# Kernel optimization log

Hardware: AMD Instinct MI355X
Metric: run time of the kernel (lower is better)

The kernel has to match this reference:

```python
import jax, jax.numpy as jnp
import numpy as np

B, S, D, H = 2, 2048, 1024, 16
DK = D // H


def setup_inputs() -> dict:
    key = jax.random.key(0)
    ks = jax.random.split(key, 12)
    s = 0.02
    return {
        "q": jax.random.normal(ks[0], (B, S, D), jnp.float32),
        "k": jax.random.normal(ks[1], (B, S, D), jnp.float32),
        "v": jax.random.normal(ks[2], (B, S, D), jnp.float32),
        "mask": jax.random.randint(ks[3], (1, 1, S, S), 0, 2, jnp.int32),
        "Wq": jax.random.normal(ks[4], (D, D), jnp.float32) * s,
        "bq": jnp.zeros((D,), jnp.float32),
        "Wk": jax.random.normal(ks[5], (D, D), jnp.float32) * s,
        "bk": jnp.zeros((D,), jnp.float32),
        "Wv": jax.random.normal(ks[6], (D, D), jnp.float32) * s,
        "bv": jnp.zeros((D,), jnp.float32),
        "Wo": jax.random.normal(ks[7], (D, D), jnp.float32) * s,
        "bo": jnp.zeros((D,), jnp.float32),
    }


def reference(q, k, v, mask, Wq, bq, Wk, bk, Wv, bv, Wo, bo):
    # linear projections (torch Linear: x @ W.T + b)
    qp = q @ Wq.T + bq
    kp = k @ Wk.T + bk
    vp = v @ Wv.T + bv
    # [B, S, D] -> [B, H, S, DK]
    split = lambda x: x.reshape(B, S, H, DK).transpose(0, 2, 1, 3)
    qh, kh, vh = split(qp), split(kp), split(vp)
    scale = 1.0 / jnp.sqrt(jnp.float32(DK))
    attn = jnp.einsum('bhsd,bhtd->bhst', qh, kh) * scale  # [B,H,S,S]
    attn = jnp.where(mask == 0, jnp.float32(-1e9), attn)
    attn = jax.nn.softmax(attn, axis=-1)
    out = jnp.einsum('bhst,bhtd->bhsd', attn, vh)  # [B,H,S,DK]
    concat = out.transpose(0, 2, 1, 3).reshape(B, S, D)
    return concat @ Wo.T + bo
```

## Files before the change

kernel.cpp:

```cpp
#include <hip/hip_runtime.h>
#include <hip/hip_bf16.h>


using bf16x8 = __attribute__((ext_vector_type(8))) short;
using f32x4  = __attribute__((ext_vector_type(4))) float;

constexpr int Bc = 2, Sc = 2048, Dc = 1024, Hc = 16, DKc = 64;
constexpr int Mc = Bc * Sc;
#define QSCALE 0.18033688011112042f

__device__ __forceinline__ void lds_load16(const void* g, void* l) {
  __builtin_amdgcn_global_load_lds(
      (const __attribute__((address_space(1))) unsigned int*)g,
      (__attribute__((address_space(3))) unsigned int*)l, 16, 0, 0);
}

#if __has_builtin(__builtin_amdgcn_exp2f)
__device__ __forceinline__ float exp2_fast(float x) { return __builtin_amdgcn_exp2f(x); }
#else
__device__ __forceinline__ float exp2_fast(float x) {
  float r;
  asm("v_exp_f32 %0, %1\n\ts_nop 0" : "=v"(r) : "v"(x));
  return r;
}
#endif

__device__ __forceinline__ unsigned pack_trunc(float a, float b) {
  return __builtin_amdgcn_perm(__float_as_uint(b), __float_as_uint(a), 0x07060302u);
}

__device__ __forceinline__ unsigned pack2bf(float a, float b) {
  union { __hip_bfloat16 h; unsigned short s; } ua, ub;
  ua.h = __float2bfloat16(a);
  ub.h = __float2bfloat16(b);
  return (unsigned)ua.s | ((unsigned)ub.s << 16);
}

__global__ void prep(const float* __restrict__ q, const float* __restrict__ k,
                     const float* __restrict__ v, const int* __restrict__ mask,
                     const float* __restrict__ Wq, const float* __restrict__ Wk,
                     const float* __restrict__ Wv, const float* __restrict__ Wo,
                     char* __restrict__ ws) {
  const size_t MB = 1024 * 1024;
  int blk = blockIdx.x;
  if (blk < 12288) {
    int which = blk >> 12;
    int i = (((blk & 4095) << 8) + threadIdx.x) * 4;
    const float* s = which == 0 ? q : (which == 1 ? k : v);
    __hip_bfloat16* d = (__hip_bfloat16*)(ws + (size_t)which * 8 * MB);
    float4 x = *(const float4*)&s[i];
    uint2 pk = {pack2bf(x.x, x.y), pack2bf(x.z, x.w)};
    *(uint2*)&d[i] = pk;
  } else if (blk < 16384) {
    int bb = blk - 12288;
    int which = bb >> 10;
    int i = (((bb & 1023) << 8) + threadIdx.x) * 4;
    const float* s = which == 0 ? Wq : (which == 1 ? Wk : (which == 2 ? Wv : Wo));
    __hip_bfloat16* d = which < 3 ? (__hip_bfloat16*)(ws + (24 + 2 * which) * MB)
                                  : (__hip_bfloat16*)(ws + 30 * MB);
    float4 x = *(const float4*)&s[i];
    uint2 pk = {pack2bf(x.x, x.y), pack2bf(x.z, x.w)};
    *(uint2*)&d[i] = pk;
  } else {
    int i = ((blk - 16384) << 8) + threadIdx.x;
    unsigned long long bal = __ballot(mask[i] != 0);
    if ((threadIdx.x & 63) == 0)
      ((unsigned long long*)(ws + 32 * MB))[i >> 6] = bal;
  }
}

__global__ __launch_bounds__(256, 3) void proj_qkv(
    const __hip_bfloat16* __restrict__ qb, const __hip_bfloat16* __restrict__ kb,
    const __hip_bfloat16* __restrict__ vb, const __hip_bfloat16* __restrict__ Wcat,
    const float* __restrict__ bq, const float* __restrict__ bk,
    const float* __restrict__ bv, __hip_bfloat16* __restrict__ qhd,
    __hip_bfloat16* __restrict__ khd, __hip_bfloat16* __restrict__ vtd) {
  __shared__ __align__(16) __hip_bfloat16 As[2][128 * 32];
  __shared__ __align__(16) __hip_bfloat16 Bs[2][128 * 32];
  const int tid = threadIdx.x;
  const int f = blockIdx.x, g = f >> 3;
  const int m0 = ((f & 7) * 4 + g / 24) * 128;
  const int n0 = (g % 24) * 128;
  const int which = n0 >> 10, nl0 = n0 & 1023;
  const __hip_bfloat16* X = which == 0 ? qb : (which == 1 ? kb : vb);
  const float* bias = which == 0 ? bq : (which == 1 ? bk : bv);
  const int w = tid >> 6, lane = tid & 63, ln = lane & 15, quad = lane >> 4;
  const int rl = w * 32 + (lane >> 2);
  const int sw8 = ((lane & 3) ^ ((lane >> 2) & 3)) * 8;
  const int aoff = (n0 + rl) * 1024 + sw8;
  const int boff = (m0 + rl) * 1024 + sw8;
  char* aDst = (char*)As + w * 2048 + lane * 16;
  char* bDst = (char*)Bs + w * 2048 + lane * 16;
  const int rkq = (quad ^ (ln & 3)) * 16;
  const int rA0 = ((w >> 1) * 64 + ln) * 64 + rkq;
  const int rB0 = ((w & 1) * 64 + ln) * 64 + rkq;
  f32x4 acc[4][4] = {};

#define PSTAGE(KO, BI)                                                        \
  {                                                                           \
    lds_load16(&Wcat[aoff + (KO)], aDst + (BI)*8192);                         \
    lds_load16(&Wcat[aoff + 16384 + (KO)], aDst + (BI)*8192 + 1024);          \
    lds_load16(&X[boff + (KO)], bDst + (BI)*8192);                            \
    lds_load16(&X[boff + 16384 + (KO)], bDst + (BI)*8192 + 1024);             \
  }

  PSTAGE(0, 0);
  if (which == 2) {
    for (int kb32 = 0; kb32 < 32; ++kb32) {
      const int bi = kb32 & 1;
      __syncthreads();
      if (kb32 < 31) PSTAGE((kb32 + 1) * 32, bi ^ 1);
      bf16x8 af[4], bf[4];
#pragma unroll
      for (int i = 0; i < 4; ++i)
        af[i] = *(bf16x8*)((char*)As + bi * 8192 + rA0 + i * 1024);
#pragma unroll
      for (int j = 0; j < 4; ++j)
        bf[j] = *(bf16x8*)((char*)Bs + bi * 8192 + rB0 + j * 1024);
#pragma unroll
      for (int i = 0; i < 4; ++i)
#pragma unroll
        for (int j = 0; j < 4; ++j)
          acc[i][j] = __builtin_amdgcn_mfma_f32_16x16x32_bf16(bf[j], af[i],
                                                              acc[i][j], 0, 0, 0);
    }
  } else {
    for (int kb32 = 0; kb32 < 32; ++kb32) {
      const int bi = kb32 & 1;
      __syncthreads();
      if (kb32 < 31) PSTAGE((kb32 + 1) * 32, bi ^ 1);
      bf16x8 af[4], bf[4];
#pragma unroll
      for (int i = 0; i < 4; ++i)
        af[i] = *(bf16x8*)((char*)As + bi * 8192 + rA0 + i * 1024);
#pragma unroll
      for (int j = 0; j < 4; ++j)
        bf[j] = *(bf16x8*)((char*)Bs + bi * 8192 + rB0 + j * 1024);
#pragma unroll
      for (int i = 0; i < 4; ++i)
#pragma unroll
        for (int j = 0; j < 4; ++j)
          acc[i][j] = __builtin_amdgcn_mfma_f32_16x16x32_bf16(af[i], bf[j],
                                                              acc[i][j], 0, 0, 0);
    }
  }

  const int wA = (w >> 1) * 64, wB = (w & 1) * 64;
  if (which == 2) {
#pragma unroll
    for (int i = 0; i < 4; ++i) {
      int nf = nl0 + wA + i * 16 + ln;
      int h = nf >> 6, dk = nf & 63;
      float bb = bias[nf];
#pragma unroll
      for (int j = 0; j < 4; ++j) {
        int sb = m0 + wB + j * 16 + quad * 4;
        int b = sb >> 11, s = sb & 2047;
        float vv[4] = {acc[i][j][0] + bb, acc[i][j][1] + bb,
                       acc[i][j][2] + bb, acc[i][j][3] + bb};
        uint2 pk = {pack2bf(vv[0], vv[1]), pack2bf(vv[2], vv[3])};
        *(uint2*)&vtd[(((size_t)(b * Hc + h) * DKc + dk) * Sc) + s] = pk;
      }
    }
  } else {
#pragma unroll
    for (int i = 0; i < 4; ++i) {
      int nfb = nl0 + wA + i * 16 + quad * 4;
      float4 b4 = *(const float4*)&bias[nfb];
      int h = nfb >> 6, dk0 = nfb & 63;
#pragma unroll
      for (int j = 0; j < 4; ++j) {
        int sg = m0 + wB + j * 16 + ln;
        int b = sg >> 11, s = sg & 2047;
        float vv[4] = {acc[i][j][0] + b4.x, acc[i][j][1] + b4.y,
                       acc[i][j][2] + b4.z, acc[i][j][3] + b4.w};
        if (which == 0) {
          uint2 pk = {pack2bf(vv[0] * QSCALE, vv[1] * QSCALE),
                      pack2bf(vv[2] * QSCALE, vv[3] * QSCALE)};
          *(uint2*)&qhd[(((size_t)(b * Hc + h) * Sc + s) * DKc) + dk0] = pk;
        } else {
          uint2 pk = {pack2bf(vv[0], vv[1]), pack2bf(vv[2], vv[3])};
          *(uint2*)&khd[(((size_t)(b * Hc + h) * Sc + s) * DKc) + dk0] = pk;
        }
      }
    }
  }
}

__global__ __launch_bounds__(256, 2) void gemm_out(
    const __hip_bfloat16* __restrict__ X, const __hip_bfloat16* __restrict__ W,
    const float* __restrict__ bias, float* __restrict__ Y) {
  __shared__ __align__(16) __hip_bfloat16 As[2][64 * 64];
  __shared__ __align__(16) __hip_bfloat16 Bs[2][128 * 64];
  const int tid = threadIdx.x;
  const int f = blockIdx.x, g = f >> 3;
  const int m0 = ((f & 7) * 4 + (g >> 4)) * 128;
  const int n0 = (g & 15) * 64;
  const int w = tid >> 6, lane = tid & 63, ln = lane & 15, quad = lane >> 4;
  const int wA = (w & 1) * 32, wB = (w >> 1) * 64;
  const int swz = ((lane & 7) ^ (lane >> 3)) * 8;
  const int rk0 = ln * 128 + ((quad ^ (ln & 7)) * 16);
  const int rk1 = ln * 128 + (((quad + 4) ^ (ln & 7)) * 16);
  const int aoff = (n0 + w * 16 + (lane >> 3)) * 1024 + swz;
  const int boff = (m0 + w * 32 + (lane >> 3)) * 1024 + swz;
  f32x4 acc[2][4] = {};

#define OSTAGE(KO, BI)                                                        \
  {                                                                           \
    _Pragma("unroll") for (int i = 0; i < 2; ++i)                             \
        lds_load16(&W[aoff + i * 8192 + (KO)],                                \
                   (char*)As[BI] + w * 2048 + lane * 16 + i * 1024);          \
    _Pragma("unroll") for (int i = 0; i < 4; ++i)                             \
        lds_load16(&X[boff + i * 8192 + (KO)],                                \
                   (char*)Bs[BI] + w * 4096 + lane * 16 + i * 1024);          \
  }

  OSTAGE(0, 0);
  for (int kb64 = 0; kb64 < 16; ++kb64) {
    const int bi = kb64 & 1;
    __syncthreads();
    if (kb64 + 1 < 16) OSTAGE((kb64 + 1) * 64, bi ^ 1);
    bf16x8 af[2][2], bf[4][2];
#pragma unroll
    for (int i = 0; i < 2; ++i) {
      af[i][0] = *(bf16x8*)((char*)As[bi] + wA * 128 + i * 2048 + rk0);
      af[i][1] = *(bf16x8*)((char*)As[bi] + wA * 128 + i * 2048 + rk1);
    }
#pragma unroll
    for (int j = 0; j < 4; ++j) {
      bf[j][0] = *(bf16x8*)((char*)Bs[bi] + wB * 128 + j * 2048 + rk0);
      bf[j][1] = *(bf16x8*)((char*)Bs[bi] + wB * 128 + j * 2048 + rk1);
    }
#pragma unroll
    for (int i = 0; i < 2; ++i)
#pragma unroll
      for (int j = 0; j < 4; ++j) {
        acc[i][j] = __builtin_amdgcn_mfma_f32_16x16x32_bf16(af[i][0], bf[j][0],
                                                            acc[i][j], 0, 0, 0);
        acc[i][j] = __builtin_amdgcn_mfma_f32_16x16x32_bf16(af[i][1], bf[j][1],
                                                            acc[i][j], 0, 0, 0);
      }
  }
#pragma unroll
  for (int i = 0; i < 2; ++i) {
    int nfb = n0 + wA + i * 16 + quad * 4;
    float4 b4 = *(const float4*)&bias[nfb];
#pragma unroll
    for (int j = 0; j < 4; ++j) {
      int sg = m0 + wB + j * 16 + ln;
      float4 st = {acc[i][j][0] + b4.x, acc[i][j][1] + b4.y,
                   acc[i][j][2] + b4.z, acc[i][j][3] + b4.w};
      *(float4*)&Y[(size_t)sg * Dc + nfb] = st;
    }
  }
}

__global__ __launch_bounds__(512, 4) void flash_attn(
    const __hip_bfloat16* __restrict__ qh, const __hip_bfloat16* __restrict__ kh,
    const __hip_bfloat16* __restrict__ vt, const uint4* __restrict__ mb4,
    __hip_bfloat16* __restrict__ oc) {
  __shared__ __align__(16) char L[51200];
  const int tid = threadIdx.x;
  const int f = blockIdx.x, g = f >> 3;
  const int bh = (f & 7) * 4 + (g >> 4);
  const int q0 = (g & 15) * 128;
  const int b = bh >> 4, h = bh & 15;
  const int w = tid >> 6, lane = tid & 63, ln = lane & 15, quad = lane >> 4;
  const int qg = w >> 1, kg = w & 1;
  const size_t base = (size_t)bh * Sc * DKc;
  const __hip_bfloat16* khb = kh + base;
  const __hip_bfloat16* vtb = vt + base;

  bf16x8 qf[2][2];
#pragma unroll
  for (int qt = 0; qt < 2; ++qt)
#pragma unroll
    for (int kc = 0; kc < 2; ++kc)
      qf[qt][kc] = *(const bf16x8*)&qh[base +
          (size_t)(q0 + qg * 32 + qt * 16 + ln) * 64 + kc * 32 + quad * 8];

  bf16x8 onesA;
#pragma unroll
  for (int i = 0; i < 8; ++i) onesA[i] = (short)0x3F80;

  const int swz = ((lane & 7) ^ (lane >> 3)) * 8;
  const int rk0 = ln * 128 + ((quad ^ (ln & 7)) * 16);
  const int rk1 = ln * 128 + (((quad + 4) ^ (ln & 7)) * 16);
  const int rkv = ln * 128 + ((((kg << 2) + quad) ^ (ln & 7)) * 16);
  const int rPw = 32768 + qg * 4608 + ln * 144 + kg * 64 + quad * 8;
  const int rPb = 32768 + qg * 4608 + ln * 144 + kg * 64 + quad * 16;
  char* dmaL = L + w * 1024 + lane * 16;
  int koff = (w * 8 + (lane >> 3)) * 64 + swz;
  int voff = (w * 8 + (lane >> 3)) * Sc + swz;
  int midx0 = (q0 + qg * 32 + ln) * 16;
  int midx1 = midx0 + 256;
  const int sh0 = quad * 4, sh1 = quad * 4 + 16;

#define KV_DMA(BI)                                                            \
  {                                                                           \
    lds_load16(khb + koff, dmaL + (BI)*8192);                                 \
    lds_load16(vtb + voff, dmaL + 16384 + (BI)*8192);                         \
  }

  f32x4 Oacc[4][2] = {};
  f32x4 lacc[2] = {};
  KV_DMA(0);

#define FTILE(BUF, E0, E1)                                                    \
  {                                                                           \
    bf16x8 kf[2][2];                                                          \
    _Pragma("unroll") for (int tl = 0; tl < 2; ++tl) {                        \
      kf[tl][0] = *(bf16x8*)(L + (BUF)*8192 + (kg * 2 + tl) * 2048 + rk0);    \
      kf[tl][1] = *(bf16x8*)(L + (BUF)*8192 + (kg * 2 + tl) * 2048 + rk1);    \
    }                                                                         \
    _Pragma("unroll") for (int qt = 0; qt < 2; ++qt) {                        \
      f32x4 s4[2];                                                            \
      __builtin_amdgcn_s_setprio(1);                                          \
      _Pragma("unroll") for (int tl = 0; tl < 2; ++tl) {                      \
        f32x4 z = {0.f, 0.f, 0.f, 0.f};                                       \
        z = __builtin_amdgcn_mfma_f32_16x16x32_bf16(kf[tl][0], qf[qt][0], z,  \
                                                    0, 0, 0);                 \
        s4[tl] = __builtin_amdgcn_mfma_f32_16x16x32_bf16(kf[tl][1],           \
                                                         qf[qt][1], z, 0, 0, 0); \
      }                                                                       \
      __builtin_amdgcn_s_setprio(0);                                          \
      unsigned word = qt ? (E1) : (E0);                                       \
      _Pragma("unroll") for (int tl = 0; tl < 2; ++tl) {                      \
        unsigned pre = word >> (tl ? sh1 : sh0);                              \
        float p[4];                                                           \
        _Pragma("unroll") for (int r = 0; r < 4; ++r) {                       \
          float e = exp2_fast(s4[tl][r]);                                     \
          p[r] = (pre & (1u << r)) ? e : 0.f;                                 \
        }                                                                     \
        uint2 pk = {pack_trunc(p[0], p[1]), pack_trunc(p[2], p[3])};          \
        *(uint2*)(L + rPw + qt * 2304 + tl * 32) = pk;                        \
      }                                                                       \
    }                                                                         \
    bf16x8 vf[4], pb[2];                                                      \
    _Pragma("unroll") for (int dt = 0; dt < 4; ++dt)                          \
        vf[dt] = *(bf16x8*)(L + 16384 + (BUF)*8192 + dt * 2048 + rkv);        \
    _Pragma("unroll") for (int qt = 0; qt < 2; ++qt)                          \
        pb[qt] = *(bf16x8*)(L + rPb + qt * 2304);                             \
    __builtin_amdgcn_s_setprio(1);                                            \
    _Pragma("unroll") for (int qt = 0; qt < 2; ++qt)                          \
        lacc[qt] = __builtin_amdgcn_mfma_f32_16x16x32_bf16(onesA, pb[qt],     \
                                                           lacc[qt], 0, 0, 0); \
    _Pragma("unroll") for (int dt = 0; dt < 4; ++dt)                          \
        _Pragma("unroll") for (int qt = 0; qt < 2; ++qt)                      \
            Oacc[dt][qt] = __builtin_amdgcn_mfma_f32_16x16x32_bf16(           \
                vf[dt], pb[qt], Oacc[dt][qt], 0, 0, 0);                       \
    __builtin_amdgcn_s_setprio(0);                                            \
  }

  for (int it2 = 0; it2 < 16; ++it2) {
    __syncthreads();
    uint4 mq0 = mb4[midx0], mq1 = mb4[midx1];
    ++midx0; ++midx1;
    koff += 4096; voff += 64;
    KV_DMA(1);
    FTILE(0, kg ? mq0.y : mq0.x, kg ? mq1.y : mq1.x);
    __syncthreads();
    if (it2 < 15) {
      koff += 4096; voff += 64;
      KV_DMA(0);
    }
    FTILE(1, kg ? mq0.w : mq0.z, kg ? mq1.w : mq1.z);
  }

  __syncthreads();
  if (kg) {
#pragma unroll
    for (int dt = 0; dt < 4; ++dt)
#pragma unroll
      for (int qt = 0; qt < 2; ++qt) {
        int slot = (dt * 4 + quad) ^ ln;
        *(f32x4*)(L + qg * 8192 + (qt * 16 + ln) * 256 + slot * 16) =
            Oacc[dt][qt];
      }
    if (quad == 0) {
      *(float*)(L + 32768 + qg * 4608 + ln * 144 + 128) = lacc[0][0];
      *(float*)(L + 32768 + qg * 4608 + 2304 + ln * 144 + 128) = lacc[1][0];
    }
  }
  __syncthreads();
  if (!kg) {
    float linv[2];
#pragma unroll
    for (int qt = 0; qt < 2; ++qt) {
      float lsum = lacc[qt][0] +
                   *(float*)(L + 32768 + qg * 4608 + qt * 2304 + ln * 144 + 128);
      linv[qt] = 1.f / fmaxf(lsum, 1e-30f);
    }
#pragma unroll
    for (int dt = 0; dt < 4; ++dt)
#pragma unroll
      for (int qt = 0; qt < 2; ++qt) {
        int slot = (dt * 4 + quad) ^ ln;
        f32x4 part =
            *(f32x4*)(L + qg * 8192 + (qt * 16 + ln) * 256 + slot * 16);
        f32x4 o = Oacc[dt][qt];
        o[0] += part[0]; o[1] += part[1]; o[2] += part[2]; o[3] += part[3];
        uint2 pk = {pack2bf(o[0] * linv[qt], o[1] * linv[qt]),
                    pack2bf(o[2] * linv[qt], o[3] * linv[qt])};
        *(uint2*)(L + rPw + qt * 2304 + dt * 32) = pk;
      }
    __builtin_amdgcn_s_waitcnt(0);
#pragma unroll
    for (int chunk = 0; chunk < 4; ++chunk) {
      int row = chunk * 8 + (lane >> 3);
      bf16x8 val =
          *(bf16x8*)(L + 32768 + qg * 4608 + row * 144 + (lane & 7) * 16);
      int s = q0 + qg * 32 + row;
      *(bf16x8*)&oc[(size_t)(b * Sc + s) * Dc + h * 64 + (lane & 7) * 8] = val;
    }
  }
#undef KV_DMA
#undef FTILE
}

extern "C" void kernel_launch(void* const* d_in, const int* in_sizes, int n_in,
                              void* d_out, int out_size, void* d_ws, size_t ws_size,
                              hipStream_t stream) {
  const float* q  = (const float*)d_in[0];
  const float* k  = (const float*)d_in[1];
  const float* v  = (const float*)d_in[2];
  const int* mask = (const int*)d_in[3];
  const float* Wq = (const float*)d_in[4];
  const float* bq = (const float*)d_in[5];
  const float* Wk = (const float*)d_in[6];
  const float* bk = (const float*)d_in[7];
  const float* Wv = (const float*)d_in[8];
  const float* bv = (const float*)d_in[9];
  const float* Wo = (const float*)d_in[10];
  const float* bo = (const float*)d_in[11];

  char* ws = (char*)d_ws;
  const size_t MB = 1024 * 1024;
  __hip_bfloat16* qb   = (__hip_bfloat16*)(ws + 0 * MB);
  __hip_bfloat16* kb   = (__hip_bfloat16*)(ws + 8 * MB);
  __hip_bfloat16* vb   = (__hip_bfloat16*)(ws + 16 * MB);
  __hip_bfloat16* Wcat = (__hip_bfloat16*)(ws + 24 * MB);
  __hip_bfloat16* Wob  = (__hip_bfloat16*)(ws + 30 * MB);
  uint4*          mb4  = (uint4*)(ws + 32 * MB);
  __hip_bfloat16* qhd  = (__hip_bfloat16*)(ws + 33 * MB);
  __hip_bfloat16* khd  = (__hip_bfloat16*)(ws + 41 * MB);
  __hip_bfloat16* vtd  = (__hip_bfloat16*)(ws + 49 * MB);
  __hip_bfloat16* oc   = (__hip_bfloat16*)(ws + 57 * MB);

  prep<<<32768, 256, 0, stream>>>(q, k, v, mask, Wq, Wk, Wv, Wo, ws);
  proj_qkv<<<768, 256, 0, stream>>>(qb, kb, vb, Wcat, bq, bk, bv, qhd, khd, vtd);
  flash_attn<<<512, 512, 0, stream>>>(qhd, khd, vtd, mb4, oc);
  gemm_out<<<512, 256, 0, stream>>>(oc, Wob, bo, (float*)d_out);
}
```

Before: 244.7 us.

## Triple-buffer K/V tiles in flash attention with two-deep async prefetch

```diff
diff --git a/kernel.cpp b/kernel.cpp
--- a/kernel.cpp
+++ b/kernel.cpp
@@ -259,7 +259,7 @@
     const __hip_bfloat16* __restrict__ qh, const __hip_bfloat16* __restrict__ kh,
     const __hip_bfloat16* __restrict__ vt, const uint4* __restrict__ mb4,
     __hip_bfloat16* __restrict__ oc) {
-  __shared__ __align__(16) char L[51200];
+  __shared__ __align__(16) char L[67584];
   const int tid = threadIdx.x;
   const int f = blockIdx.x, g = f >> 3;
   const int bh = (f & 7) * 4 + (g >> 4);
@@ -287,8 +287,8 @@
   const int rk0 = ln * 128 + ((quad ^ (ln & 7)) * 16);
   const int rk1 = ln * 128 + (((quad + 4) ^ (ln & 7)) * 16);
   const int rkv = ln * 128 + ((((kg << 2) + quad) ^ (ln & 7)) * 16);
-  const int rPw = 32768 + qg * 4608 + ln * 144 + kg * 64 + quad * 8;
-  const int rPb = 32768 + qg * 4608 + ln * 144 + kg * 64 + quad * 16;
+  const int rPw = 49152 + qg * 4608 + ln * 144 + kg * 64 + quad * 8;
+  const int rPb = 49152 + qg * 4608 + ln * 144 + kg * 64 + quad * 16;
   char* dmaL = L + w * 1024 + lane * 16;
   int koff = (w * 8 + (lane >> 3)) * 64 + swz;
   int voff = (w * 8 + (lane >> 3)) * Sc + swz;
@@ -296,22 +296,33 @@
   int midx1 = midx0 + 256;
   const int sh0 = quad * 4, sh1 = quad * 4 + 16;
 
-#define KV_DMA(BI)                                                            \
-  {                                                                           \
-    lds_load16(khb + koff, dmaL + (BI)*8192);                                 \
-    lds_load16(vtb + voff, dmaL + 16384 + (BI)*8192);                         \
+#define KV_DMA(BOFF)                                                          \
+  {                                                                           \
+    lds_load16(khb + koff, dmaL + (BOFF));                                    \
+    lds_load16(vtb + voff, dmaL + 24576 + (BOFF));                            \
+    koff += 4096; voff += 64;                                                 \
+  }
+
+#define WB2()                                                                 \
+  {                                                                           \
+    asm volatile("s_waitcnt vmcnt(2)" ::: "memory");                          \
+    __builtin_amdgcn_s_barrier();                                             \
+  }
+#define WB0()                                                                 \
+  {                                                                           \
+    asm volatile("s_waitcnt vmcnt(0)" ::: "memory");                          \
+    __builtin_amdgcn_s_barrier();                                             \
   }
 
   f32x4 Oacc[4][2] = {};
   f32x4 lacc[2] = {};
-  KV_DMA(0);
-
-#define FTILE(BUF, E0, E1)                                                    \
+
+#define FTILE(COFF, E0, E1)                                                   \
   {                                                                           \
     bf16x8 kf[2][2];                                                          \
     _Pragma("unroll") for (int tl = 0; tl < 2; ++tl) {                        \
-      kf[tl][0] = *(bf16x8*)(L + (BUF)*8192 + (kg * 2 + tl) * 2048 + rk0);    \
-      kf[tl][1] = *(bf16x8*)(L + (BUF)*8192 + (kg * 2 + tl) * 2048 + rk1);    \
+      kf[tl][0] = *(bf16x8*)(L + (COFF) + (kg * 2 + tl) * 2048 + rk0);        \
+      kf[tl][1] = *(bf16x8*)(L + (COFF) + (kg * 2 + tl) * 2048 + rk1);        \
     }                                                                         \
     _Pragma("unroll") for (int qt = 0; qt < 2; ++qt) {                        \
       f32x4 s4[2];                                                            \
@@ -338,7 +349,7 @@
     }                                                                         \
     bf16x8 vf[4], pb[2];                                                      \
     _Pragma("unroll") for (int dt = 0; dt < 4; ++dt)                          \
-        vf[dt] = *(bf16x8*)(L + 16384 + (BUF)*8192 + dt * 2048 + rkv);        \
+        vf[dt] = *(bf16x8*)(L + 24576 + (COFF) + dt * 2048 + rkv);            \
     _Pragma("unroll") for (int qt = 0; qt < 2; ++qt)                          \
         pb[qt] = *(bf16x8*)(L + rPb + qt * 2304);                             \
     __builtin_amdgcn_s_setprio(1);                                            \
@@ -352,19 +363,33 @@
     __builtin_amdgcn_s_setprio(0);                                            \
   }
 
+  uint4 mqC0 = mb4[midx0], mqC1 = mb4[midx1];
+  ++midx0; ++midx1;
+  KV_DMA(0);
+  KV_DMA(8192);
+  int curoff = 0, preoff = 16384;
+
   for (int it2 = 0; it2 < 16; ++it2) {
-    __syncthreads();
-    uint4 mq0 = mb4[midx0], mq1 = mb4[midx1];
-    ++midx0; ++midx1;
-    koff += 4096; voff += 64;
-    KV_DMA(1);
-    FTILE(0, kg ? mq0.y : mq0.x, kg ? mq1.y : mq1.x);
-    __syncthreads();
+    uint4 mqN0, mqN1;
+    WB2();
     if (it2 < 15) {
-      koff += 4096; voff += 64;
-      KV_DMA(0);
-    }
-    FTILE(1, kg ? mq0.w : mq0.z, kg ? mq1.w : mq1.z);
+      mqN0 = mb4[midx0]; mqN1 = mb4[midx1];
+      ++midx0; ++midx1;
+      KV_DMA(preoff);
+      preoff = preoff == 16384 ? 0 : preoff + 8192;
+    }
+    FTILE(curoff, kg ? mqC0.y : mqC0.x, kg ? mqC1.y : mqC1.x);
+    curoff = curoff == 16384 ? 0 : curoff + 8192;
+    if (it2 < 15) {
+      WB2();
+      KV_DMA(preoff);
+      preoff = preoff == 16384 ? 0 : preoff + 8192;
+    } else {
+      WB0();
+    }
+    FTILE(curoff, kg ? mqC0.w : mqC0.z, kg ? mqC1.w : mqC1.z);
+    curoff = curoff == 16384 ? 0 : curoff + 8192;
+    if (it2 < 15) { mqC0 = mqN0; mqC1 = mqN1; }
   }
 
   __syncthreads();
@@ -378,8 +403,8 @@
             Oacc[dt][qt];
       }
     if (quad == 0) {
-      *(float*)(L + 32768 + qg * 4608 + ln * 144 + 128) = lacc[0][0];
-      *(float*)(L + 32768 + qg * 4608 + 2304 + ln * 144 + 128) = lacc[1][0];
+      *(float*)(L + 49152 + qg * 4608 + ln * 144 + 128) = lacc[0][0];
+      *(float*)(L + 49152 + qg * 4608 + 2304 + ln * 144 + 128) = lacc[1][0];
     }
   }
   __syncthreads();
@@ -388,7 +413,7 @@
 #pragma unroll
     for (int qt = 0; qt < 2; ++qt) {
       float lsum = lacc[qt][0] +
-                   *(float*)(L + 32768 + qg * 4608 + qt * 2304 + ln * 144 + 128);
+                   *(float*)(L + 49152 + qg * 4608 + qt * 2304 + ln * 144 + 128);
       linv[qt] = 1.f / fmaxf(lsum, 1e-30f);
     }
 #pragma unroll
@@ -409,13 +434,15 @@
     for (int chunk = 0; chunk < 4; ++chunk) {
       int row = chunk * 8 + (lane >> 3);
       bf16x8 val =
-          *(bf16x8*)(L + 32768 + qg * 4608 + row * 144 + (lane & 7) * 16);
+          *(bf16x8*)(L + 49152 + qg * 4608 + row * 144 + (lane & 7) * 16);
       int s = q0 + qg * 32 + row;
       *(bf16x8*)&oc[(size_t)(b * Sc + s) * Dc + h * 64 + (lane & 7) * 8] = val;
     }
   }
 #undef KV_DMA
 #undef FTILE
+#undef WB2
+#undef WB0
 }
 
 extern "C" void kernel_launch(void* const* d_in, const int* in_sizes, int n_in,
```

After: 244.9 us. Within noise of the previous version (+0.1%).
